# Kernel tuning notes

Hardware: AMD Instinct MI355X
Metric: run time of the kernel (lower is better)

The kernel has to match this reference:

```python
import jax, jax.numpy as jnp
import numpy as np

SEP_THRESHOLD = 5.0
TEMPERATURE = 0.1          # sigmoid temperature
SCALING_FACTOR = 1.0
DIST_TEMPERATURE = 1.0     # exponential temperature for repulsion energy
ATT_LOSS_GATE = 0.0
REP_LOSS_GATE = 0.0
EPS = 1e-10


def setup_inputs() -> dict:
    key = jax.random.key(0)
    k1, k2 = jax.random.split(key)
    B, L, K, C, D = 16, 64, 32, 32, 512
    prior = jax.random.normal(k1, (B, L, K, C), dtype=jnp.float32)
    h = jax.random.normal(k2, (B, L, D), dtype=jnp.float32)
    return {"prior": prior, "h": h}


def _jsd_matrix(prior):
    # prior: (B, L, K, C) logits -> pairwise JSD summed over K factors: (B, L, L)
    logp = jax.nn.log_softmax(prior, axis=-1)          # (B,L,K,C)
    p = jnp.exp(logp)
    p1, p2 = p[:, :, None], p[:, None]                  # (B,L,1,K,C), (B,1,L,K,C)
    lp1, lp2 = logp[:, :, None], logp[:, None]
    logm = jnp.log(0.5 * (p1 + p2))                     # mixture log-probs
    kl_p_m = jnp.sum(p1 * (lp1 - logm), axis=-1)        # (B,L,L,K)
    kl_q_m = jnp.sum(p2 * (lp2 - logm), axis=-1)
    jsd = 0.5 * (kl_p_m + kl_q_m)
    return jsd.sum(axis=-1) * SCALING_FACTOR            # (B,L,L)


def _ste_mask(soft, hard, triu):
    # straight-through: hard values forward, soft gradient backward
    return (hard + soft - jax.lax.stop_gradient(soft)) * triu


def reference(prior, h):
    B, L, K, C = prior.shape
    jsd = _jsd_matrix(prior)                            # (B,L,L)

    triu = jnp.triu(jnp.ones((L, L), dtype=prior.dtype), k=1)
    soft_att = jax.nn.sigmoid((SEP_THRESHOLD - jsd) / TEMPERATURE)
    hard_att = (jsd < SEP_THRESHOLD).astype(prior.dtype)
    att_mask = _ste_mask(soft_att, hard_att, triu)
    soft_rep = jax.nn.sigmoid((jsd - SEP_THRESHOLD) / TEMPERATURE)
    hard_rep = (jsd >= SEP_THRESHOLD).astype(prior.dtype)
    rep_mask = _ste_mask(soft_rep, hard_rep, triu)

    # pairwise MSE over hidden dim: (B,L,L)
    diff = h[:, :, None, :] - h[:, None, :, :]
    pairwise_mse = jnp.mean(diff * diff, axis=-1)

    loss_att = (pairwise_mse * att_mask).sum() / (att_mask.sum() + EPS)
    loss_att = jnp.where(loss_att > ATT_LOSS_GATE, loss_att, 0.0)

    repulsion_energy = jnp.exp(-pairwise_mse / DIST_TEMPERATURE)
    loss_rep = (repulsion_energy * rep_mask).sum() / (rep_mask.sum() + EPS)
    loss_rep = jnp.where(loss_rep > REP_LOSS_GATE, loss_rep, 0.0)

    return loss_att, loss_rep
```

## Files before the change

### kernel.cpp

```cpp
#include <hip/hip_runtime.h>
#include <math.h>

#define NB 16
#define NL 64
#define NK 32
#define NC 32
#define ND 512
#define EPSF 1e-10f

#define TILES_PER_B 36
#define PAIR_BLOCKS (NB * TILES_PER_B * 2)

#define THRS 14.426950408889634f
#define L2E  1.4426950408889634f

typedef _Float16 half2v __attribute__((ext_vector_type(2)));
typedef _Float16 half4v __attribute__((ext_vector_type(4)));
typedef _Float16 half8v __attribute__((ext_vector_type(8)));


__global__ void __launch_bounds__(256) softmax_kernel(
        const float* __restrict__ prior,
        const float* __restrict__ hg,
        _Float16* __restrict__ P,
        float2* __restrict__ H2,
        _Float16* __restrict__ h16) {
    int bl = blockIdx.x;
    int t  = threadIdx.x;

    const float* src = prior + (size_t)bl * (NK * NC);
    float4 x = *(const float4*)(src + t * 4);
    float y0 = x.x * L2E, y1 = x.y * L2E, y2 = x.z * L2E, y3 = x.w * L2E;

    float m = fmaxf(fmaxf(y0, y1), fmaxf(y2, y3));
    #pragma unroll
    for (int w = 4; w >= 1; w >>= 1)
        m = fmaxf(m, __shfl_xor(m, w, 8));

    float e0 = exp2f(y0 - m), e1 = exp2f(y1 - m);
    float e2 = exp2f(y2 - m), e3 = exp2f(y3 - m);
    float s = e0 + e1 + e2 + e3;
    #pragma unroll
    for (int w = 4; w >= 1; w >>= 1)
        s += __shfl_xor(s, w, 8);

    float rs = 1.0f / s;
    float ls = __log2f(s);
    float p0 = e0 * rs, p1 = e1 * rs, p2 = e2 * rs, p3 = e3 * rs;
    float l0 = (y0 - m) - ls, l1 = (y1 - m) - ls;
    float l2 = (y2 - m) - ls, l3 = (y3 - m) - ls;

    half4v pv;
    pv[0] = (_Float16)fmaxf(p0, 1e-6f);
    pv[1] = (_Float16)fmaxf(p1, 1e-6f);
    pv[2] = (_Float16)fmaxf(p2, 1e-6f);
    pv[3] = (_Float16)fmaxf(p3, 1e-6f);
    *(half4v*)(P + (size_t)bl * (NK * NC) + t * 4) = pv;

    float2 hv = *(const float2*)(hg + (size_t)bl * ND + t * 2);
    half2v hh; hh[0] = (_Float16)hv.x; hh[1] = (_Float16)hv.y;
    *(half2v*)(h16 + (size_t)bl * ND + t * 2) = hh;

    float hacc = p0 * l0 + p1 * l1 + p2 * l2 + p3 * l3;
    #pragma unroll
    for (int w = 32; w >= 1; w >>= 1)
        hacc += __shfl_xor(hacc, w);
    __shared__ float red[4];
    int lane = t & 63, wib = t >> 6;
    if (lane == 0) red[wib] = hacc;
    __syncthreads();
    if (t == 0)
        H2[bl] = make_float2(red[0] + red[1], red[2] + red[3]);
}

__device__ __forceinline__ float bf4(float v0, float v1, float v2, float v3,
                                     bool hi32, bool hi16) {
    float sel0 = hi32 ? v2 : v0, oth0 = hi32 ? v0 : v2;
    float sel1 = hi32 ? v3 : v1, oth1 = hi32 ? v1 : v3;
    float w0 = sel0 + __shfl_xor(oth0, 32);
    float w1 = sel1 + __shfl_xor(oth1, 32);
    float sel = hi16 ? w1 : w0, oth = hi16 ? w0 : w1;
    float x = sel + __shfl_xor(oth, 16);
    x += __shfl_xor(x, 8);
    x += __shfl_xor(x, 4);
    x += __shfl_xor(x, 2);
    x += __shfl_xor(x, 1);
    return x;
}

__global__ void __launch_bounds__(256) pair_kernel(
        const _Float16* __restrict__ P,
        const float2* __restrict__ H2g,
        const _Float16* __restrict__ h16,
        float* __restrict__ partials) {
    __shared__ _Float16 sPj[8][1024];
    __shared__ _Float16 sHj[8][512];
    __shared__ float2 sh2j[8];
    __shared__ float red[4][4];

    int tid  = threadIdx.x;
    int lane = tid & 63;
    int wv   = tid >> 6;

    int wg    = blockIdx.x;
    int b     = wg / (TILES_PER_B * 2);
    int rem72 = wg % (TILES_PER_B * 2);
    int t36   = rem72 >> 1;
    int half  = rem72 & 1;

    int ti = 0, rem = t36;
    while (rem >= 8 - ti) { rem -= 8 - ti; ++ti; }
    int tj = ti + rem;
    bool diag = (ti == tj);
    int bi0 = b * NL + ti * 8;
    int bj0 = b * NL + tj * 8;

    int r = half * 4 + wv;

    const _Float16* arow = P + (size_t)(bi0 + r) * (NK * NC);
    half8v ar1 = *(const half8v*)(arow + lane * 8);
    half8v ar2 = *(const half8v*)(arow + 512 + lane * 8);
    half8v hr  = *(const half8v*)(h16 + (size_t)(bi0 + r) * ND + lane * 8);
    float2 h2i = H2g[bi0 + r];

    {
        const float4* sp = (const float4*)(P + (size_t)bj0 * (NK * NC));
        float4* dp = (float4*)&sPj[0][0];
        #pragma unroll
        for (int k = 0; k < 4; ++k) dp[tid + 256 * k] = sp[tid + 256 * k];
        const float4* sh = (const float4*)(h16 + (size_t)bj0 * ND);
        float4* dh = (float4*)&sHj[0][0];
        dh[tid] = sh[tid]; dh[tid + 256] = sh[tid + 256];
    }
    if (tid < 8) sh2j[tid] = H2g[bj0 + tid];
    __syncthreads();

    bool hi32 = (lane & 32) != 0;
    bool hi16 = (lane & 16) != 0;
    int  sgrp = lane >> 4;

    float attN = 0.0f, attC = 0.0f, repN = 0.0f, repC = 0.0f;

    #pragma unroll
    for (int sb = 0; sb < 8; sb += 4) {
        float S[4], M[4];
        #pragma unroll
        for (int q = 0; q < 4; ++q) {
            int s = sb + q;
            half8v b1 = *(const half8v*)&sPj[s][lane * 8];
            half8v t1 = ar1 + b1;
            float a0 = 0.f, a1 = 0.f;
            #pragma unroll
            for (int e = 0; e < 8; e += 2) {
                float f0 = (float)t1[e];     a0 = fmaf(f0, __log2f(f0), a0);
                float f1 = (float)t1[e + 1]; a1 = fmaf(f1, __log2f(f1), a1);
            }
            S[q] = a0 + a1;

            half8v hs = *(const half8v*)&sHj[s][lane * 8];
            half8v d = hr - hs;
            float m0 = 0.f, m1 = 0.f;
            #pragma unroll
            for (int e = 0; e < 8; e += 2) {
                m0 = fmaf((float)d[e],     (float)d[e],     m0);
                m1 = fmaf((float)d[e + 1], (float)d[e + 1], m1);
            }
            M[q] = m0 + m1;
        }

        float xSA = bf4(S[0], S[1], S[2], S[3], hi32, hi16);
        float xM  = bf4(M[0], M[1], M[2], M[3], hi32, hi16);

        int smine = sb + sgrp;
        float2 h2j = sh2j[smine];
        float statA = h2i.x + h2j.x + 32.0f - xSA;
        bool valid = (!diag) || (smine > r);
        float stat = statA;

        if (__any(valid && (statA < THRS))) {
            float SB[4];
            #pragma unroll
            for (int q = 0; q < 4; ++q) {
                int s = sb + q;
                half8v b2 = *(const half8v*)&sPj[s][512 + lane * 8];
                half8v t2 = ar2 + b2;
                float a0 = 0.f, a1 = 0.f;
                #pragma unroll
                for (int e = 0; e < 8; e += 2) {
                    float g0 = (float)t2[e];     a0 = fmaf(g0, __log2f(g0), a0);
                    float g1 = (float)t2[e + 1]; a1 = fmaf(g1, __log2f(g1), a1);
                }
                SB[q] = a0 + a1;
            }
            float xSB = bf4(SB[0], SB[1], SB[2], SB[3], hi32, hi16);
            stat = statA + (h2i.y + h2j.y + 32.0f - xSB);
        }

        float mse   = xM * (1.0f / ND);
        float rterm = exp2f(-mse * L2E);
        bool act   = ((lane & 15) == 0) && valid;
        bool isAtt = stat < THRS;
        attN += (act && isAtt)  ? mse   : 0.0f;
        attC += (act && isAtt)  ? 1.0f  : 0.0f;
        repN += (act && !isAtt) ? rterm : 0.0f;
        repC += (act && !isAtt) ? 1.0f  : 0.0f;
    }

    attN += __shfl_xor(attN, 16); attN += __shfl_xor(attN, 32);
    attC += __shfl_xor(attC, 16); attC += __shfl_xor(attC, 32);
    repN += __shfl_xor(repN, 16); repN += __shfl_xor(repN, 32);
    repC += __shfl_xor(repC, 16); repC += __shfl_xor(repC, 32);

    if (lane == 0) {
        red[wv][0] = attN; red[wv][1] = attC;
        red[wv][2] = repN; red[wv][3] = repC;
    }
    __syncthreads();
    if (tid < 4) {
        float v = red[0][tid] + red[1][tid] + red[2][tid] + red[3][tid];
        partials[blockIdx.x * 4 + tid] = v;
    }
}

__global__ void __launch_bounds__(256) finalize_kernel(
        const float* __restrict__ partials,
        float* __restrict__ out) {
    int tid = threadIdx.x;
    float a0 = 0.0f, a1 = 0.0f, a2 = 0.0f, a3 = 0.0f;
    for (int bkt = tid; bkt < PAIR_BLOCKS; bkt += 256) {
        a0 += partials[bkt * 4 + 0];
        a1 += partials[bkt * 4 + 1];
        a2 += partials[bkt * 4 + 2];
        a3 += partials[bkt * 4 + 3];
    }
    #pragma unroll
    for (int w = 32; w >= 1; w >>= 1) {
        a0 += __shfl_xor(a0, w);
        a1 += __shfl_xor(a1, w);
        a2 += __shfl_xor(a2, w);
        a3 += __shfl_xor(a3, w);
    }
    __shared__ float red[4][4];
    int lane = tid & 63, wib = tid >> 6;
    if (lane == 0) {
        red[wib][0] = a0; red[wib][1] = a1; red[wib][2] = a2; red[wib][3] = a3;
    }
    __syncthreads();
    if (tid == 0) {
        float s0 = red[0][0] + red[1][0] + red[2][0] + red[3][0];
        float s1 = red[0][1] + red[1][1] + red[2][1] + red[3][1];
        float s2 = red[0][2] + red[1][2] + red[2][2] + red[3][2];
        float s3 = red[0][3] + red[1][3] + red[2][3] + red[3][3];
        float la = s0 / (s1 + EPSF);
        float lr = s2 / (s3 + EPSF);
        out[0] = (la > 0.0f) ? la : 0.0f;
        out[1] = (lr > 0.0f) ? lr : 0.0f;
    }
}

extern "C" void kernel_launch(void* const* d_in, const int* in_sizes, int n_in,
                              void* d_out, int out_size, void* d_ws, size_t ws_size,
                              hipStream_t stream) {
    const float* prior = (const float*)d_in[0];
    const float* h     = (const float*)d_in[1];
    float* out = (float*)d_out;
    float* ws  = (float*)d_ws;

    float* partials = ws;
    _Float16* P = (_Float16*)(ws + 8192);
    float2* H2 = (float2*)(ws + 8192 + 524288);
    _Float16* h16 = (_Float16*)(ws + 8192 + 524288 + 2048);

    softmax_kernel<<<NB * NL, 256, 0, stream>>>(prior, h, P, H2, h16);

    pair_kernel<<<PAIR_BLOCKS, 256, 0, stream>>>(P, H2, h16, partials);

    finalize_kernel<<<1, 256, 0, stream>>>(partials, out);
}
```

Before: 24.83 us.

## Remap pair kernel so each 8-lane group owns one pair, drop early-exit

The pair kernel now gives each group of 8 lanes a full (i,j) pair. Each lane covers a 128-element slice of the prior and a 64-element slice of h, and the cross-lane reductions shrink to three shuffle steps. The shared-memory rows are padded (1088/576 halves) to avoid bank conflicts. H2 is merged into one scalar per row. The second-half JSD skip (__any early exit) is removed, so every pair always evaluates all 32 factors, trading extra log work for less shuffle and reduction overhead.

```diff
diff --git a/kernel.cpp b/kernel.cpp
--- a/kernel.cpp
+++ b/kernel.cpp
@@ -23,7 +23,7 @@
         const float* __restrict__ prior,
         const float* __restrict__ hg,
         _Float16* __restrict__ P,
-        float2* __restrict__ H2,
+        float* __restrict__ H2,
         _Float16* __restrict__ h16) {
     int bl = blockIdx.x;
     int t  = threadIdx.x;
@@ -69,33 +69,16 @@
     int lane = t & 63, wib = t >> 6;
     if (lane == 0) red[wib] = hacc;
     __syncthreads();
-    if (t == 0)
-        H2[bl] = make_float2(red[0] + red[1], red[2] + red[3]);
-}
-
-__device__ __forceinline__ float bf4(float v0, float v1, float v2, float v3,
-                                     bool hi32, bool hi16) {
-    float sel0 = hi32 ? v2 : v0, oth0 = hi32 ? v0 : v2;
-    float sel1 = hi32 ? v3 : v1, oth1 = hi32 ? v1 : v3;
-    float w0 = sel0 + __shfl_xor(oth0, 32);
-    float w1 = sel1 + __shfl_xor(oth1, 32);
-    float sel = hi16 ? w1 : w0, oth = hi16 ? w0 : w1;
-    float x = sel + __shfl_xor(oth, 16);
-    x += __shfl_xor(x, 8);
-    x += __shfl_xor(x, 4);
-    x += __shfl_xor(x, 2);
-    x += __shfl_xor(x, 1);
-    return x;
+    if (t == 0) H2[bl] = red[0] + red[1] + red[2] + red[3];
 }
 
 __global__ void __launch_bounds__(256) pair_kernel(
         const _Float16* __restrict__ P,
-        const float2* __restrict__ H2g,
+        const float* __restrict__ H2g,
         const _Float16* __restrict__ h16,
         float* __restrict__ partials) {
-    __shared__ _Float16 sPj[8][1024];
-    __shared__ _Float16 sHj[8][512];
-    __shared__ float2 sh2j[8];
+    __shared__ _Float16 sPj[8 * 1088];
+    __shared__ _Float16 sHj[8 * 576];
     __shared__ float red[4][4];
 
     int tid  = threadIdx.x;
@@ -115,101 +98,92 @@
     int bi0 = b * NL + ti * 8;
     int bj0 = b * NL + tj * 8;
 
+    {
+        const _Float16* srcP = P + (size_t)bj0 * (NK * NC);
+        #pragma unroll
+        for (int it = 0; it < 4; ++it) {
+            int c = tid + 256 * it;
+            int row = c >> 7, sg = (c >> 4) & 7, idx = c & 15;
+            half8v v = *(const half8v*)(srcP + row * 1024 + sg * 128 + idx * 8);
+            *(half8v*)(sPj + row * 1088 + sg * 136 + idx * 8) = v;
+        }
+        const _Float16* srcH = h16 + (size_t)bj0 * ND;
+        #pragma unroll
+        for (int it = 0; it < 2; ++it) {
+            int c = tid + 256 * it;
+            int row = c >> 6, sg = (c >> 3) & 7, idx = c & 7;
+            half8v v = *(const half8v*)(srcH + row * 512 + sg * 64 + idx * 8);
+            *(half8v*)(sHj + row * 576 + sg * 72 + idx * 8) = v;
+        }
+    }
+    __syncthreads();
+
+    int q = lane & 7;
+    int g = lane >> 3;
     int r = half * 4 + wv;
 
-    const _Float16* arow = P + (size_t)(bi0 + r) * (NK * NC);
-    half8v ar1 = *(const half8v*)(arow + lane * 8);
-    half8v ar2 = *(const half8v*)(arow + 512 + lane * 8);
-    half8v hr  = *(const half8v*)(h16 + (size_t)(bi0 + r) * ND + lane * 8);
-    float2 h2i = H2g[bi0 + r];
-
-    {
-        const float4* sp = (const float4*)(P + (size_t)bj0 * (NK * NC));
-        float4* dp = (float4*)&sPj[0][0];
-        #pragma unroll
-        for (int k = 0; k < 4; ++k) dp[tid + 256 * k] = sp[tid + 256 * k];
-        const float4* sh = (const float4*)(h16 + (size_t)bj0 * ND);
-        float4* dh = (float4*)&sHj[0][0];
-        dh[tid] = sh[tid]; dh[tid + 256] = sh[tid + 256];
-    }
-    if (tid < 8) sh2j[tid] = H2g[bj0 + tid];
-    __syncthreads();
-
-    bool hi32 = (lane & 32) != 0;
-    bool hi16 = (lane & 16) != 0;
-    int  sgrp = lane >> 4;
-
-    float attN = 0.0f, attC = 0.0f, repN = 0.0f, repC = 0.0f;
-
-    #pragma unroll
-    for (int sb = 0; sb < 8; sb += 4) {
-        float S[4], M[4];
-        #pragma unroll
-        for (int q = 0; q < 4; ++q) {
-            int s = sb + q;
-            half8v b1 = *(const half8v*)&sPj[s][lane * 8];
-            half8v t1 = ar1 + b1;
-            float a0 = 0.f, a1 = 0.f;
-            #pragma unroll
-            for (int e = 0; e < 8; e += 2) {
-                float f0 = (float)t1[e];     a0 = fmaf(f0, __log2f(f0), a0);
-                float f1 = (float)t1[e + 1]; a1 = fmaf(f1, __log2f(f1), a1);
-            }
-            S[q] = a0 + a1;
-
-            half8v hs = *(const half8v*)&sHj[s][lane * 8];
-            half8v d = hr - hs;
-            float m0 = 0.f, m1 = 0.f;
-            #pragma unroll
-            for (int e = 0; e < 8; e += 2) {
-                m0 = fmaf((float)d[e],     (float)d[e],     m0);
-                m1 = fmaf((float)d[e + 1], (float)d[e + 1], m1);
-            }
-            M[q] = m0 + m1;
-        }
-
-        float xSA = bf4(S[0], S[1], S[2], S[3], hi32, hi16);
-        float xM  = bf4(M[0], M[1], M[2], M[3], hi32, hi16);
-
-        int smine = sb + sgrp;
-        float2 h2j = sh2j[smine];
-        float statA = h2i.x + h2j.x + 32.0f - xSA;
-        bool valid = (!diag) || (smine > r);
-        float stat = statA;
-
-        if (__any(valid && (statA < THRS))) {
-            float SB[4];
-            #pragma unroll
-            for (int q = 0; q < 4; ++q) {
-                int s = sb + q;
-                half8v b2 = *(const half8v*)&sPj[s][512 + lane * 8];
-                half8v t2 = ar2 + b2;
-                float a0 = 0.f, a1 = 0.f;
-                #pragma unroll
-                for (int e = 0; e < 8; e += 2) {
-                    float g0 = (float)t2[e];     a0 = fmaf(g0, __log2f(g0), a0);
-                    float g1 = (float)t2[e + 1]; a1 = fmaf(g1, __log2f(g1), a1);
-                }
-                SB[q] = a0 + a1;
-            }
-            float xSB = bf4(SB[0], SB[1], SB[2], SB[3], hi32, hi16);
-            stat = statA + (h2i.y + h2j.y + 32.0f - xSB);
-        }
-
-        float mse   = xM * (1.0f / ND);
-        float rterm = exp2f(-mse * L2E);
-        bool act   = ((lane & 15) == 0) && valid;
-        bool isAtt = stat < THRS;
-        attN += (act && isAtt)  ? mse   : 0.0f;
-        attC += (act && isAtt)  ? 1.0f  : 0.0f;
-        repN += (act && !isAtt) ? rterm : 0.0f;
-        repC += (act && !isAtt) ? 1.0f  : 0.0f;
-    }
-
-    attN += __shfl_xor(attN, 16); attN += __shfl_xor(attN, 32);
-    attC += __shfl_xor(attC, 16); attC += __shfl_xor(attC, 32);
-    repN += __shfl_xor(repN, 16); repN += __shfl_xor(repN, 32);
-    repC += __shfl_xor(repC, 16); repC += __shfl_xor(repC, 32);
+    bool valid = (!diag) || (g > r);
+
+    const _Float16* arow = P   + (size_t)(bi0 + r) * (NK * NC) + q * 128;
+    const _Float16* hrow = h16 + (size_t)(bi0 + r) * ND + q * 64;
+    const _Float16* sPg  = sPj + g * 1088 + q * 136;
+    const _Float16* sHg  = sHj + g * 576  + q * 72;
+
+    float h2i = H2g[bi0 + r];
+    float h2j = H2g[bj0 + g];
+
+    float S0 = 0.f, S1 = 0.f;
+    #pragma unroll
+    for (int e = 0; e < 16; ++e) {
+        half8v a  = *(const half8v*)(arow + e * 8);
+        half8v bb = *(const half8v*)(sPg + e * 8);
+        half8v t  = a + bb;
+        #pragma unroll
+        for (int u = 0; u < 8; u += 2) {
+            float f0 = (float)t[u];     S0 = fmaf(f0, __log2f(f0), S0);
+            float f1 = (float)t[u + 1]; S1 = fmaf(f1, __log2f(f1), S1);
+        }
+    }
+    float S = S0 + S1;
+
+    float M0 = 0.f, M1 = 0.f;
+    #pragma unroll
+    for (int e = 0; e < 8; ++e) {
+        half8v x = *(const half8v*)(hrow + e * 8);
+        half8v y = *(const half8v*)(sHg + e * 8);
+        half8v d = x - y;
+        #pragma unroll
+        for (int u = 0; u < 8; u += 2) {
+            M0 = fmaf((float)d[u],     (float)d[u],     M0);
+            M1 = fmaf((float)d[u + 1], (float)d[u + 1], M1);
+        }
+    }
+    float M = M0 + M1;
+
+    #pragma unroll
+    for (int m = 1; m <= 4; m <<= 1) {
+        S += __shfl_xor(S, m);
+        M += __shfl_xor(M, m);
+    }
+
+    float stat  = h2i + h2j + 64.0f - S;
+    float mse   = M * (1.0f / ND);
+    float rterm = exp2f(-mse * L2E);
+    bool act    = (q == 0) && valid;
+    bool isAtt  = stat < THRS;
+
+    float attN = (act && isAtt)  ? mse   : 0.0f;
+    float attC = (act && isAtt)  ? 1.0f  : 0.0f;
+    float repN = (act && !isAtt) ? rterm : 0.0f;
+    float repC = (act && !isAtt) ? 1.0f  : 0.0f;
+
+    #pragma unroll
+    for (int m = 8; m <= 32; m <<= 1) {
+        attN += __shfl_xor(attN, m);
+        attC += __shfl_xor(attC, m);
+        repN += __shfl_xor(repN, m);
+        repC += __shfl_xor(repC, m);
+    }
 
     if (lane == 0) {
         red[wv][0] = attN; red[wv][1] = attC;
@@ -268,8 +242,8 @@
 
     float* partials = ws;
     _Float16* P = (_Float16*)(ws + 8192);
-    float2* H2 = (float2*)(ws + 8192 + 524288);
-    _Float16* h16 = (_Float16*)(ws + 8192 + 524288 + 2048);
+    float* H2 = ws + 8192 + 524288;
+    _Float16* h16 = (_Float16*)(ws + 8192 + 524288 + 1024);
 
     softmax_kernel<<<NB * NL, 256, 0, stream>>>(prior, h, P, H2, h16);
 
```

Result: slower. 30.95 us (+24.6%).
